# Optimization experiments

Measured on AMD Instinct MI355X. Metric: run time of the kernel, lower is better.

Reference implementation:

```python
import jax, jax.numpy as jnp
import numpy as np

EPS = 1e-5
N_HEADS = 8

def _layernorm(h, g, b):
    mu = jnp.mean(h, axis=-1, keepdims=True)
    var = jnp.mean((h - mu) ** 2, axis=-1, keepdims=True)
    return g * (h - mu) * jax.lax.rsqrt(var + EPS) + b

def _mlp_ln(x, W1, b1, W2, b2, g, beta):
    # Linear -> SiLU -> Linear -> LayerNorm (torch nn.Sequential processor)
    h = jax.nn.silu(x @ W1.T + b1)
    h = h @ W2.T + b2
    return _layernorm(h, g, beta)

def setup_inputs() -> dict:
    key = jax.random.key(0)
    ks = jax.random.split(key, 16)
    B, S, D = 4, 2048, 1024
    M, P, C = 128, 256, 512
    def lin(k, o, i):
        return (jax.random.normal(k, (o, i), jnp.float32) / np.sqrt(i)).astype(jnp.float32)
    inp = {}
    inp['x'] = jax.random.normal(ks[0], (B, S, D), jnp.float32)
    inp['scale_types'] = jax.random.randint(ks[1], (B, S), 0, 3)
    for name, dim, k1, k2 in [('mol', M, 2, 3), ('path', P, 4, 5), ('cell', C, 6, 7)]:
        inp[name + '_W1'] = lin(ks[k1], dim, D)
        inp[name + '_b1'] = jnp.zeros((dim,), jnp.float32)
        inp[name + '_W2'] = lin(ks[k2], dim, dim)
        inp[name + '_b2'] = jnp.zeros((dim,), jnp.float32)
        inp[name + '_g'] = jnp.ones((dim,), jnp.float32)
        inp[name + '_beta'] = jnp.zeros((dim,), jnp.float32)
    inp['int_W1'] = lin(ks[8], D, M + P + C)
    inp['int_b1'] = jnp.zeros((D,), jnp.float32)
    inp['int_W2'] = lin(ks[9], D, D)
    inp['int_b2'] = jnp.zeros((D,), jnp.float32)
    inp['int_g'] = jnp.ones((D,), jnp.float32)
    inp['int_beta'] = jnp.zeros((D,), jnp.float32)
    inp['attn_Wqkv'] = lin(ks[10], 3 * D, D)
    inp['attn_bqkv'] = jnp.zeros((3 * D,), jnp.float32)
    inp['attn_Wo'] = lin(ks[11], D, D)
    inp['attn_bo'] = jnp.zeros((D,), jnp.float32)
    inp['scale_w'] = jnp.ones((3,), jnp.float32) / 3.0
    return inp

def reference(x, scale_types,
              mol_W1, mol_b1, mol_W2, mol_b2, mol_g, mol_beta,
              path_W1, path_b1, path_W2, path_b2, path_g, path_beta,
              cell_W1, cell_b1, cell_W2, cell_b2, cell_g, cell_beta,
              int_W1, int_b1, int_W2, int_b2, int_g, int_beta,
              attn_Wqkv, attn_bqkv, attn_Wo, attn_bo, scale_w):
    B, S, D = x.shape
    # per-token routing: each token goes through exactly one expert; the
    # other two scale outputs are zeros (mask instead of Python loop).
    mol = _mlp_ln(x, mol_W1, mol_b1, mol_W2, mol_b2, mol_g, mol_beta) * (scale_types == 0)[..., None]
    path = _mlp_ln(x, path_W1, path_b1, path_W2, path_b2, path_g, path_beta) * (scale_types == 1)[..., None]
    cell = _mlp_ln(x, cell_W1, cell_b1, cell_W2, cell_b2, cell_g, cell_beta) * (scale_types == 2)[..., None]
    cat = jnp.concatenate([mol, path, cell], axis=-1)  # [B,S,M+P+C]
    integrated = _layernorm(jax.nn.silu(cat @ int_W1.T + int_b1) @ int_W2.T + int_b2, int_g, int_beta)
    # torch nn.MultiheadAttention (batch_first, self-attention)
    Dh = D // N_HEADS
    qkv = integrated @ attn_Wqkv.T + attn_bqkv  # [B,S,3D]
    q, k, v = jnp.split(qkv, 3, axis=-1)
    q = q.reshape(B, S, N_HEADS, Dh)
    k = k.reshape(B, S, N_HEADS, Dh)
    v = v.reshape(B, S, N_HEADS, Dh)
    scores = jnp.einsum('bqhd,bkhd->bhqk', q, k) / np.sqrt(Dh).astype(np.float32)
    attn = jax.nn.softmax(scores, axis=-1)
    o = jnp.einsum('bhqk,bkhd->bqhd', attn, v).reshape(B, S, D)
    attended = o @ attn_Wo.T + attn_bo
    w = jax.nn.softmax(scale_w, axis=0)
    final = integrated + w[0] * attended
    return (final, mol, path, cell)
```

## Files before the change

### kernel.cpp

```cpp
#include <hip/hip_runtime.h>
#include <cstdint>
#include <cstddef>

typedef unsigned short u16;
typedef unsigned int u32;
typedef short bf16x8 __attribute__((ext_vector_type(8)));
typedef float f32x4 __attribute__((ext_vector_type(4)));

__device__ __forceinline__ float bf2f(u16 u){
  union { u32 i; float f; } c; c.i = ((u32)u) << 16; return c.f;
}
__device__ __forceinline__ u16 f2bf(float f){
  union { float f; u32 i; } c; c.f = f;
  u32 r = c.i + 0x7FFFu + ((c.i >> 16) & 1u);
  return (u16)(r >> 16);
}
__device__ __forceinline__ void gload_lds16(const void* g, void* l){
  __builtin_amdgcn_global_load_lds(
      (const __attribute__((address_space(1))) u32*)g,
      (__attribute__((address_space(3))) u32*)l, 16, 0, 0);
}

struct ConvArgs {
  const float* src[11];
  u16* dst[11];
  u32 base[12];
};
__global__ __launch_bounds__(256)
void f32_to_bf16_multi(ConvArgs a){
  u32 i = blockIdx.x * 256 + threadIdx.x;
  if (i >= a.base[11]) return;
  int j = 0;
  #pragma unroll
  for (int k = 1; k < 11; ++k) j += (i >= a.base[k]);
  u32 li = i - a.base[j];
  const float4* s = (const float4*)a.src[j] + (size_t)li * 2;
  float4 va = s[0], vb = s[1];
  u16 o[8] = {f2bf(va.x),f2bf(va.y),f2bf(va.z),f2bf(va.w),
              f2bf(vb.x),f2bf(vb.y),f2bf(vb.z),f2bf(vb.w)};
  *(uint4*)(a.dst[j] + (size_t)li * 8) = *(const uint4*)o;
}

__global__ __launch_bounds__(256)
void concat3_f32(const float* __restrict__ a, const float* __restrict__ b,
                 const float* __restrict__ c, float* __restrict__ d){
  int i = blockIdx.x * 256 + threadIdx.x;
  if (i < 128) d[i] = a[i];
  else if (i < 384) d[i] = b[i - 128];
  else if (i < 896) d[i] = c[i - 384];
}

template<int EPI>
__device__ __forceinline__ void gemm_body(
    const u16* __restrict__ A, const u16* __restrict__ W,
    const float* __restrict__ bias, void* __restrict__ Cv,
    int N, int K, int lda, int ldc,
    const u16* __restrict__ I, const float* __restrict__ sw,
    int bx, int by)
{
  __shared__ __align__(16) u16 As[128*64];
  __shared__ __align__(16) u16 Bs[128*64];
  const int tid  = threadIdx.x;
  const int lane = tid & 63;
  const int wave = tid >> 6;
  const int wr = wave >> 1, wc = wave & 1;
  const int m0 = by * 128, n0 = bx * 128;

  f32x4 acc[4][4];
  #pragma unroll
  for (int r=0;r<4;++r)
    #pragma unroll
    for (int c=0;c<4;++c)
      #pragma unroll
      for (int e=0;e<4;++e) acc[r][c][e] = 0.f;

  int srow[4], soff[4];
  #pragma unroll
  for (int j=0;j<4;++j){
    int rr = (wave*4 + j)*8 + (lane>>3);
    srow[j] = rr;
    soff[j] = ((lane & 7) ^ (rr & 7)) * 8;
  }

  for (int k0 = 0; k0 < K; k0 += 64){
    #pragma unroll
    for (int j=0;j<4;++j){
      gload_lds16(A + (size_t)(m0 + srow[j])*lda + k0 + soff[j], As + (wave*4+j)*512);
      gload_lds16(W + (size_t)(n0 + srow[j])*K   + k0 + soff[j], Bs + (wave*4+j)*512);
    }
    __syncthreads();
    #pragma unroll
    for (int ks=0; ks<2; ++ks){
      bf16x8 af[4], bfr[4];
      #pragma unroll
      for (int r=0;r<4;++r){
        int row = wr*64 + r*16 + (lane&15);
        int cs  = (ks*4 + (lane>>4)) ^ (row & 7);
        af[r] = *(const bf16x8*)(As + row*64 + cs*8);
      }
      #pragma unroll
      for (int c=0;c<4;++c){
        int row = wc*64 + c*16 + (lane&15);
        int cs  = (ks*4 + (lane>>4)) ^ (row & 7);
        bfr[c] = *(const bf16x8*)(Bs + row*64 + cs*8);
      }
      #pragma unroll
      for (int r=0;r<4;++r)
        #pragma unroll
        for (int c=0;c<4;++c)
          acc[r][c] = __builtin_amdgcn_mfma_f32_16x16x32_bf16(af[r], bfr[c], acc[r][c], 0,0,0);
    }
    __syncthreads();
  }

  float w0 = 0.f;
  if (EPI == 2){
    float s0 = sw[0], s1 = sw[1], s2 = sw[2];
    float mx = fmaxf(s0, fmaxf(s1, s2));
    float e0 = __expf(s0-mx), e1 = __expf(s1-mx), e2 = __expf(s2-mx);
    w0 = e0 / (e0 + e1 + e2);
  }
  u16*   C16 = (u16*)Cv;
  float* C32 = (float*)Cv;
  #pragma unroll
  for (int c=0;c<4;++c){
    int col = n0 + wc*64 + c*16 + (lane&15);
    float bv = bias[col];
    #pragma unroll
    for (int r=0;r<4;++r){
      int rbase = m0 + wr*64 + r*16 + (lane>>4)*4;
      #pragma unroll
      for (int e=0;e<4;++e){
        int row = rbase + e;
        float v = acc[r][c][e] + bv;
        if (EPI == 1) v = v / (1.f + __expf(-v));
        if (EPI == 2){
          v = bf2f(I[(size_t)row*ldc + col]) + w0 * v;
          C32[(size_t)row*ldc + col] = v;
        } else {
          C16[(size_t)row*ldc + col] = f2bf(v);
        }
      }
    }
  }
}

template<int EPI>
__global__ __launch_bounds__(256, 2)
void gemm_bt(const u16* __restrict__ A, const u16* __restrict__ W,
             const float* __restrict__ bias, void* __restrict__ Cv,
             int N, int K, int lda, int ldc,
             const u16* __restrict__ I, const float* __restrict__ sw)
{
  gemm_body<EPI>(A, W, bias, Cv, N, K, lda, ldc, I, sw, blockIdx.x, blockIdx.y);
}

__global__ __launch_bounds__(256, 2)
void gemm_w2group(const u16* __restrict__ S1, u16* __restrict__ S2,
                  const u16* __restrict__ w0, const u16* __restrict__ w1,
                  const u16* __restrict__ w2, const float* __restrict__ b0,
                  const float* __restrict__ b1, const float* __restrict__ b2)
{
  int bx = blockIdx.x;
  if (bx < 64){
    gemm_body<0>(S1, w0, b0, S2, 128, 128, 896, 896, nullptr, nullptr, 0, bx);
  } else if (bx < 192){
    int l = bx - 64;
    gemm_body<0>(S1+128, w1, b1, S2+128, 256, 256, 896, 896, nullptr, nullptr, l>>6, l&63);
  } else {
    int l = bx - 192;
    gemm_body<0>(S1+384, w2, b2, S2+384, 512, 512, 896, 896, nullptr, nullptr, l>>6, l&63);
  }
}

template<int D>
__device__ __forceinline__ void ln_body_masked(
    u16* __restrict__ H, int ldh, const float* __restrict__ g,
    const float* __restrict__ beta, const int* __restrict__ st,
    int eid, float* __restrict__ outp)
{
  const int tid = threadIdx.x, lane = tid & 63, wave = tid >> 6;
  const int token = blockIdx.x * 4 + wave;
  constexpr int VPT = D / 64;
  float v[VPT];
  u16* row = H + (size_t)token * ldh + lane * VPT;
  #pragma unroll
  for (int i=0;i<VPT/2;++i){
    u32 u = ((const u32*)row)[i];
    v[2*i]   = bf2f((u16)(u & 0xFFFFu));
    v[2*i+1] = bf2f((u16)(u >> 16));
  }
  float s = 0.f;
  #pragma unroll
  for (int i=0;i<VPT;++i) s += v[i];
  #pragma unroll
  for (int off=1; off<64; off<<=1) s += __shfl_xor(s, off);
  float mu = s * (1.f / D);
  float q = 0.f;
  #pragma unroll
  for (int i=0;i<VPT;++i){ float d = v[i] - mu; q += d * d; }
  #pragma unroll
  for (int off=1; off<64; off<<=1) q += __shfl_xor(q, off);
  float rs = rsqrtf(q * (1.f / D) + 1e-5f);
  float msk = (st[token] == eid) ? 1.f : 0.f;
  #pragma unroll
  for (int i=0;i<VPT;++i){
    float gg = g[lane*VPT + i];
    float bb = beta[lane*VPT + i];
    float val = (gg * (v[i] - mu) * rs + bb) * msk;
    outp[(size_t)token * D + lane * VPT + i] = val;
    row[i] = f2bf(val);
  }
}

__global__ __launch_bounds__(256, 4)
void ln_expert(u16* __restrict__ S2,
               const float* __restrict__ g0, const float* __restrict__ be0,
               const float* __restrict__ g1, const float* __restrict__ be1,
               const float* __restrict__ g2, const float* __restrict__ be2,
               const int* __restrict__ st,
               float* __restrict__ o0, float* __restrict__ o1,
               float* __restrict__ o2)
{
  if (blockIdx.y == 0)      ln_body_masked<128>(S2,     896, g0, be0, st, 0, o0);
  else if (blockIdx.y == 1) ln_body_masked<256>(S2+128, 896, g1, be1, st, 1, o1);
  else                      ln_body_masked<512>(S2+384, 896, g2, be2, st, 2, o2);
}

__global__ __launch_bounds__(256, 4)
void ln_int(const u16* __restrict__ H, const float* __restrict__ g,
            const float* __restrict__ beta, u16* __restrict__ outp)
{
  const int tid = threadIdx.x, lane = tid & 63, wave = tid >> 6;
  const int token = blockIdx.x * 4 + wave;
  constexpr int D = 1024, VPT = 16;
  float v[VPT];
  const u16* row = H + (size_t)token * D + lane * VPT;
  #pragma unroll
  for (int i=0;i<VPT/2;++i){
    u32 u = ((const u32*)row)[i];
    v[2*i]   = bf2f((u16)(u & 0xFFFFu));
    v[2*i+1] = bf2f((u16)(u >> 16));
  }
  float s = 0.f;
  #pragma unroll
  for (int i=0;i<VPT;++i) s += v[i];
  #pragma unroll
  for (int off=1; off<64; off<<=1) s += __shfl_xor(s, off);
  float mu = s * (1.f / D);
  float q = 0.f;
  #pragma unroll
  for (int i=0;i<VPT;++i){ float d = v[i] - mu; q += d * d; }
  #pragma unroll
  for (int off=1; off<64; off<<=1) q += __shfl_xor(q, off);
  float rs = rsqrtf(q * (1.f / D) + 1e-5f);
  #pragma unroll
  for (int i=0;i<VPT;++i){
    float val = g[lane*VPT + i] * (v[i] - mu) * rs + beta[lane*VPT + i];
    outp[(size_t)token * D + lane * VPT + i] = f2bf(val);
  }
}

__global__ __launch_bounds__(256)
void transpose_v(const u16* __restrict__ qkv, u16* __restrict__ vt)
{
  __shared__ __align__(16) u16 T[64*72];
  const int tid = threadIdx.x;
  const int tt = blockIdx.x;
  const int dt = blockIdx.y;
  const int bh = blockIdx.z;
  const int b = bh >> 3, h = bh & 7;
  #pragma unroll
  for (int i=0;i<2;++i){
    int idx = tid + 256*i;
    int r = idx >> 3, c8 = idx & 7;
    const uint4* src = (const uint4*)(qkv + (size_t)(b*2048 + tt*64 + r)*3072
                                      + 2048 + h*128 + dt*64 + c8*8);
    *(uint4*)(T + r*72 + ((c8 ^ (r>>3)) & 7)*8) = *src;
  }
  __syncthreads();
  #pragma unroll
  for (int i=0;i<2;++i){
    int idx = tid + 256*i;
    int dr = idx >> 3, tc = idx & 7;
    u16 tmp[8];
    #pragma unroll
    for (int j=0;j<8;++j){
      int kap = tc*8 + j;
      int hp = kap >> 5, r2 = kap & 31;
      int srow = hp*32 + ((r2 & 1) ? 16 + (r2 >> 1) : (r2 >> 1));
      tmp[j] = T[srow*72 + (((dr>>3) ^ (srow>>3)) & 7)*8 + (dr & 7)];
    }
    *(uint4*)(vt + ((size_t)bh*128 + dt*64 + dr)*2048 + tt*64 + tc*8) = *(const uint4*)tmp;
  }
}

__global__ __launch_bounds__(256, 4)
void flash_attn(const u16* __restrict__ qkv, const u16* __restrict__ vt,
                u16* __restrict__ o)
{
  __shared__ __align__(16) u16 Ks[8192];
  __shared__ __align__(16) u16 Vs[8192];
  __shared__ __align__(16) u16 Ps[4*1024];
  const int tid = threadIdx.x, lane = tid & 63, wave = tid >> 6;
  const int b = blockIdx.z, h = blockIdx.y, q0 = blockIdx.x * 64;
  const float cl2   = 0.12751791892f;
  const float DEFER = 90.50966799187809f;

  bf16x8 qreg[4];
  {
    const u16* qrow = qkv + (size_t)(b*2048 + q0 + wave*16 + (lane&15))*3072
                      + h*128 + (lane>>4)*8;
    #pragma unroll
    for (int kk=0;kk<4;++kk) qreg[kk] = *(const bf16x8*)(qrow + kk*32);
  }
  asm volatile("s_waitcnt vmcnt(0)" ::: "memory");

  const u16* ksrc[4]; const u16* vsrc[4]; int cdst[4];
  #pragma unroll
  for (int i=0;i<4;++i){
    int cidx = (wave*4 + i)*64 + lane;
    int krow = cidx >> 4, kcs = cidx & 15;
    int kcsrc = (kcs & 8) | ((kcs & 7) ^ (krow & 7));
    ksrc[i] = qkv + (size_t)(b*2048 + krow)*3072 + h*128 + 1024 + kcsrc*8;
    int vd = cidx >> 3, vcs = cidx & 7;
    vsrc[i] = vt + ((size_t)(b*8 + h)*128 + vd)*2048 + (vcs ^ (vd & 7))*8;
    cdst[i] = cidx * 8;
  }

  auto stageK = [&](int kt){
    #pragma unroll
    for (int i=0;i<4;++i) gload_lds16(ksrc[i] + (size_t)kt*196608, Ks + cdst[i]);
  };
  auto stageV = [&](int kt){
    #pragma unroll
    for (int i=0;i<4;++i) gload_lds16(vsrc[i] + kt*64, Vs + cdst[i]);
  };

  f32x4 oacc[8];
  #pragma unroll
  for (int f=0;f<8;++f)
    #pragma unroll
    for (int e=0;e<4;++e) oacc[f][e] = 0.f;
  float m_run[4] = {-3e38f,-3e38f,-3e38f,-3e38f};
  float l_run[4] = {0.f,0.f,0.f,0.f};
  u16* PsW  = Ps + wave*1024;
  u32* PsW32 = (u32*)PsW;

  stageK(0);
  stageV(0);
  asm volatile("s_waitcnt vmcnt(4)" ::: "memory");
  __builtin_amdgcn_s_barrier();
  __builtin_amdgcn_sched_barrier(0);

  for (int kt=0; kt<32; ++kt){
    f32x4 s[4];
    #pragma unroll
    for (int cb=0;cb<4;++cb)
      #pragma unroll
      for (int e=0;e<4;++e) s[cb][e] = 0.f;
    __builtin_amdgcn_s_setprio(1);
    #pragma unroll
    for (int kk=0;kk<4;++kk){
      #pragma unroll
      for (int cb=0;cb<4;++cb){
        int row  = (lane&15) + 16*cb;
        int c    = kk*4 + (lane>>4);
        int slot = (c & 8) | ((c & 7) ^ (row & 7));
        bf16x8 bk = *(const bf16x8*)(Ks + row*128 + slot*8);
        s[cb] = __builtin_amdgcn_mfma_f32_16x16x32_bf16(qreg[kk], bk, s[cb], 0,0,0);
      }
    }
    __builtin_amdgcn_s_setprio(0);
    asm volatile("s_waitcnt lgkmcnt(0)" ::: "memory");
    __builtin_amdgcn_sched_barrier(0);
    __builtin_amdgcn_s_barrier();
    __builtin_amdgcn_sched_barrier(0);
    stageK((kt+1)&31);

    #pragma unroll
    for (int e=0;e<4;++e){
      float t0 = s[0][e], t1 = s[1][e], t2 = s[2][e], t3 = s[3][e];
      float lmx = fmaxf(fmaxf(t0,t1), fmaxf(t2,t3));
      if (__any(lmx > m_run[e] + DEFER)){
        float mx = lmx;
        #pragma unroll
        for (int off=1; off<16; off<<=1) mx = fmaxf(mx, __shfl_xor(mx, off));
        float mnew = fmaxf(m_run[e], mx);
        float a = exp2f((m_run[e] - mnew) * cl2);
        m_run[e] = mnew;
        l_run[e] *= a;
        #pragma unroll
        for (int f=0;f<8;++f) oacc[f][e] *= a;
      }
      float ms = m_run[e];
      float p0 = exp2f((t0 - ms)*cl2), p1 = exp2f((t1 - ms)*cl2);
      float p2 = exp2f((t2 - ms)*cl2), p3 = exp2f((t3 - ms)*cl2);
      l_run[e] += (p0 + p1) + (p2 + p3);
      u32 c01, c23;
      asm("v_cvt_pk_bf16_f32 %0, %1, %2" : "=v"(c01) : "v"(p0), "v"(p1));
      asm("v_cvt_pk_bf16_f32 %0, %1, %2" : "=v"(c23) : "v"(p2), "v"(p3));
      int prow = (lane>>4)*4 + e;
      u32* base = PsW32 + prow*32;
      int j01 = lane & 15;
      int j23 = 16 + (lane & 15);
      base[((((j01>>2) ^ (prow&7)) & 7)<<2) | (j01&3)] = c01;
      base[((((j23>>2) ^ (prow&7)) & 7)<<2) | (j23&3)] = c23;
    }

    asm volatile("s_waitcnt vmcnt(4)" ::: "memory");
    __builtin_amdgcn_sched_barrier(0);
    __builtin_amdgcn_s_barrier();
    __builtin_amdgcn_sched_barrier(0);

    __builtin_amdgcn_s_setprio(1);
    #pragma unroll
    for (int kk=0;kk<2;++kk){
      int prow = lane & 15;
      int pc   = kk*4 + (lane>>4);
      bf16x8 pa = *(const bf16x8*)(PsW + prow*64 + ((pc ^ (prow & 7)) & 7)*8);
      #pragma unroll
      for (int f=0;f<8;++f){
        int d = f*16 + (lane&15);
        int c = kk*4 + (lane>>4);
        bf16x8 vb = *(const bf16x8*)(Vs + d*64 + (c ^ (d & 7))*8);
        oacc[f] = __builtin_amdgcn_mfma_f32_16x16x32_bf16(pa, vb, oacc[f], 0,0,0);
      }
    }
    __builtin_amdgcn_s_setprio(0);
    asm volatile("s_waitcnt lgkmcnt(0) vmcnt(0)" ::: "memory");
    __builtin_amdgcn_sched_barrier(0);
    __builtin_amdgcn_s_barrier();
    __builtin_amdgcn_sched_barrier(0);
    if (kt + 1 < 32) stageV(kt+1);
  }

  #pragma unroll
  for (int e=0;e<4;++e){
    float l = l_run[e];
    #pragma unroll
    for (int off=1; off<16; off<<=1) l += __shfl_xor(l, off);
    l_run[e] = 1.f / l;
  }
  #pragma unroll
  for (int f=0;f<8;++f)
    #pragma unroll
    for (int e=0;e<4;++e){
      int row = q0 + wave*16 + (lane>>4)*4 + e;
      int col = h*128 + f*16 + (lane&15);
      o[(size_t)(b*2048 + row)*1024 + col] = f2bf(oacc[f][e] * l_run[e]);
    }
}

extern "C" void kernel_launch(void* const* d_in, const int* in_sizes, int n_in,
                              void* d_out, int out_size, void* d_ws, size_t ws_size,
                              hipStream_t stream)
{
  const float* x         = (const float*)d_in[0];
  const int*   stypes    = (const int*)d_in[1];
  const float* mol_W1    = (const float*)d_in[2];
  const float* mol_b1    = (const float*)d_in[3];
  const float* mol_W2    = (const float*)d_in[4];
  const float* mol_b2    = (const float*)d_in[5];
  const float* mol_g     = (const float*)d_in[6];
  const float* mol_beta  = (const float*)d_in[7];
  const float* path_W1   = (const float*)d_in[8];
  const float* path_b1   = (const float*)d_in[9];
  const float* path_W2   = (const float*)d_in[10];
  const float* path_b2   = (const float*)d_in[11];
  const float* path_g    = (const float*)d_in[12];
  const float* path_beta = (const float*)d_in[13];
  const float* cell_W1   = (const float*)d_in[14];
  const float* cell_b1   = (const float*)d_in[15];
  const float* cell_W2   = (const float*)d_in[16];
  const float* cell_b2   = (const float*)d_in[17];
  const float* cell_g    = (const float*)d_in[18];
  const float* cell_beta = (const float*)d_in[19];
  const float* int_W1    = (const float*)d_in[20];
  const float* int_b1    = (const float*)d_in[21];
  const float* int_W2    = (const float*)d_in[22];
  const float* int_b2    = (const float*)d_in[23];
  const float* int_g     = (const float*)d_in[24];
  const float* int_beta  = (const float*)d_in[25];
  const float* attn_Wqkv = (const float*)d_in[26];
  const float* attn_bqkv = (const float*)d_in[27];
  const float* attn_Wo   = (const float*)d_in[28];
  const float* attn_bo   = (const float*)d_in[29];
  const float* scale_w   = (const float*)d_in[30];

  float* out_final = (float*)d_out;
  float* out_mol   = out_final + 8388608;
  float* out_path  = out_mol   + 1048576;
  float* out_cell  = out_path  + 2097152;

  u16* ws    = (u16*)d_ws;
  u16* qkv   = ws;
  u16* integ = qkv   + 25165824;
  u16* S1    = integ + 8388608;
  u16* S2    = S1    + 8388608;
  u16* wb    = S2    + 8388608;
  u16* xb    = qkv;

  u16* w1f    = wb;
  u16* molW2b = w1f    + 917504;
  u16* pathW2b= molW2b + 16384;
  u16* cellW2b= pathW2b+ 65536;
  u16* intW1b = cellW2b+ 262144;
  u16* intW2b = intW1b + 917504;
  u16* qkvWb  = intW2b + 1048576;
  u16* woWb   = qkvWb  + 3145728;
  float* fbias= (float*)(woWb + 1048576);

  dim3 blk(256);

  ConvArgs ca;
  const float* srcs[11] = {x, mol_W1, path_W1, cell_W1, mol_W2, path_W2,
                           cell_W2, int_W1, int_W2, attn_Wqkv, attn_Wo};
  u16* dsts[11] = {xb, w1f, w1f + 131072, w1f + 393216, molW2b, pathW2b,
                   cellW2b, intW1b, intW2b, qkvWb, woWb};
  u32 n8s[11] = {1048576, 16384, 32768, 65536, 2048, 8192,
                 32768, 114688, 131072, 393216, 131072};
  u32 acc8 = 0;
  for (int i=0;i<11;++i){ ca.src[i]=srcs[i]; ca.dst[i]=dsts[i]; ca.base[i]=acc8; acc8+=n8s[i]; }
  ca.base[11] = acc8;
  f32_to_bf16_multi<<<(acc8 + 255)/256, blk, 0, stream>>>(ca);
  concat3_f32<<<4, blk, 0, stream>>>(mol_b1, path_b1, cell_b1, fbias);

  gemm_bt<1><<<dim3(7,64), blk, 0, stream>>>(xb, w1f, fbias, S1, 896, 1024, 1024, 896, nullptr, nullptr);
  gemm_w2group<<<448, blk, 0, stream>>>(S1, S2, molW2b, pathW2b, cellW2b,
                                        mol_b2, path_b2, cell_b2);
  ln_expert<<<dim3(2048,3), blk, 0, stream>>>(S2, mol_g, mol_beta, path_g,
                                              path_beta, cell_g, cell_beta,
                                              stypes, out_mol, out_path, out_cell);

  gemm_bt<1><<<dim3(8,64), blk, 0, stream>>>(S2, intW1b, int_b1, S1, 1024, 896,  896,  1024, nullptr, nullptr);
  gemm_bt<0><<<dim3(8,64), blk, 0, stream>>>(S1, intW2b, int_b2, S2, 1024, 1024, 1024, 1024, nullptr, nullptr);
  ln_int<<<2048, blk, 0, stream>>>(S2, int_g, int_beta, integ);

  gemm_bt<0><<<dim3(24,64), blk, 0, stream>>>(integ, qkvWb, attn_bqkv, qkv, 3072, 1024, 1024, 3072, nullptr, nullptr);
  transpose_v<<<dim3(32,2,32), blk, 0, stream>>>(qkv, S2);
  flash_attn<<<dim3(32,8,4), blk, 0, stream>>>(qkv, S2, S1);

  gemm_bt<2><<<dim3(8,64), blk, 0, stream>>>(S1, woWb, attn_bo, out_final, 1024, 1024, 1024, 1024, integ, scale_w);
}
```

Before: 329.0 us.

## Compact tokens per expert and run expert MLP GEMMs on routed rows only

A new single-block kernel builds per-expert token index lists and counts from scale_types. The expert W1 and W2 GEMMs then gather only routed rows and scatter results back, skipping tiles past each expert's count. Before, all three experts ran over every token and the results were masked afterwards. Rows for unrouted tokens in S2 are no longer written, so the masked layernorm now clamps inputs to keep stale values from producing NaN. Separately, gemm_bt remaps its block index so consecutive tiles land on the same XCD, which should improve cache locality.

```diff
diff --git a/kernel.cpp b/kernel.cpp
--- a/kernel.cpp
+++ b/kernel.cpp
@@ -42,29 +42,52 @@
 }
 
 __global__ __launch_bounds__(256)
-void concat3_f32(const float* __restrict__ a, const float* __restrict__ b,
-                 const float* __restrict__ c, float* __restrict__ d){
-  int i = blockIdx.x * 256 + threadIdx.x;
-  if (i < 128) d[i] = a[i];
-  else if (i < 384) d[i] = b[i - 128];
-  else if (i < 896) d[i] = c[i - 384];
-}
-
-template<int EPI>
+void route_compact(const int* __restrict__ st, int* __restrict__ idx,
+                   int* __restrict__ counts){
+  __shared__ int cnt[3][257];
+  const int tid = threadIdx.x;
+  int t[32];
+  #pragma unroll
+  for (int i=0;i<32;++i) t[i] = st[tid*32 + i];
+  int c0=0,c1=0,c2=0;
+  #pragma unroll
+  for (int i=0;i<32;++i){ c0 += (t[i]==0); c1 += (t[i]==1); c2 += (t[i]==2); }
+  cnt[0][tid+1]=c0; cnt[1][tid+1]=c1; cnt[2][tid+1]=c2;
+  if (tid < 3) cnt[tid][0] = 0;
+  __syncthreads();
+  if (tid < 3){
+    int acc = 0;
+    for (int i=1;i<=256;++i){ acc += cnt[tid][i]; cnt[tid][i] = acc; }
+    counts[tid] = acc;
+  }
+  __syncthreads();
+  int b0 = cnt[0][tid], b1 = cnt[1][tid], b2 = cnt[2][tid];
+  #pragma unroll
+  for (int i=0;i<32;++i){
+    int tok = tid*32 + i;
+    if (t[i]==0)      idx[b0++] = tok;
+    else if (t[i]==1) idx[8192  + b1++] = tok;
+    else              idx[16384 + b2++] = tok;
+  }
+}
+
+template<int EPI, int MODE>
 __device__ __forceinline__ void gemm_body(
     const u16* __restrict__ A, const u16* __restrict__ W,
     const float* __restrict__ bias, void* __restrict__ Cv,
     int N, int K, int lda, int ldc,
     const u16* __restrict__ I, const float* __restrict__ sw,
-    int bx, int by)
-{
+    int bx, int by, const int* __restrict__ ridx, int count)
+{
+  const int m0 = by * 128, n0 = bx * 128;
+  if (MODE && m0 >= count) return;
+
   __shared__ __align__(16) u16 As[128*64];
   __shared__ __align__(16) u16 Bs[128*64];
   const int tid  = threadIdx.x;
   const int lane = tid & 63;
   const int wave = tid >> 6;
   const int wr = wave >> 1, wc = wave & 1;
-  const int m0 = by * 128, n0 = bx * 128;
 
   f32x4 acc[4][4];
   #pragma unroll
@@ -74,19 +97,23 @@
       #pragma unroll
       for (int e=0;e<4;++e) acc[r][c][e] = 0.f;
 
-  int srow[4], soff[4];
+  int srow[4], soff[4], arow[4];
   #pragma unroll
   for (int j=0;j<4;++j){
     int rr = (wave*4 + j)*8 + (lane>>3);
     srow[j] = rr;
     soff[j] = ((lane & 7) ^ (rr & 7)) * 8;
+    int gr = m0 + rr;
+    if (MODE == 1)      arow[j] = ridx[gr < count ? gr : count-1];
+    else if (MODE == 2) arow[j] = gr < count ? gr : count-1;
+    else                arow[j] = gr;
   }
 
   for (int k0 = 0; k0 < K; k0 += 64){
     #pragma unroll
     for (int j=0;j<4;++j){
-      gload_lds16(A + (size_t)(m0 + srow[j])*lda + k0 + soff[j], As + (wave*4+j)*512);
-      gload_lds16(W + (size_t)(n0 + srow[j])*K   + k0 + soff[j], Bs + (wave*4+j)*512);
+      gload_lds16(A + (size_t)arow[j]*lda + k0 + soff[j], As + (wave*4+j)*512);
+      gload_lds16(W + (size_t)(n0 + srow[j])*K + k0 + soff[j], Bs + (wave*4+j)*512);
     }
     __syncthreads();
     #pragma unroll
@@ -134,11 +161,13 @@
         int row = rbase + e;
         float v = acc[r][c][e] + bv;
         if (EPI == 1) v = v / (1.f + __expf(-v));
+        if (MODE && row >= count) continue;
+        int crow = (MODE == 2) ? ridx[row] : row;
         if (EPI == 2){
-          v = bf2f(I[(size_t)row*ldc + col]) + w0 * v;
-          C32[(size_t)row*ldc + col] = v;
+          v = bf2f(I[(size_t)crow*ldc + col]) + w0 * v;
+          C32[(size_t)crow*ldc + col] = v;
         } else {
-          C16[(size_t)row*ldc + col] = f2bf(v);
+          C16[(size_t)crow*ldc + col] = f2bf(v);
         }
       }
     }
@@ -152,24 +181,60 @@
              int N, int K, int lda, int ldc,
              const u16* __restrict__ I, const float* __restrict__ sw)
 {
-  gemm_body<EPI>(A, W, bias, Cv, N, K, lda, ldc, I, sw, blockIdx.x, blockIdx.y);
+  int gx = gridDim.x;
+  int nwg = gx * gridDim.y;
+  int flat = blockIdx.y * gx + blockIdx.x;
+  int q = nwg >> 3;
+  int swz = (flat & 7) * q + (flat >> 3);
+  gemm_body<EPI,0>(A, W, bias, Cv, N, K, lda, ldc, I, sw,
+                   swz % gx, swz / gx, nullptr, 0);
 }
 
 __global__ __launch_bounds__(256, 2)
-void gemm_w2group(const u16* __restrict__ S1, u16* __restrict__ S2,
+void gemm_w1group(const u16* __restrict__ xb,
+                  u16* __restrict__ s1_0, u16* __restrict__ s1_1, u16* __restrict__ s1_2,
                   const u16* __restrict__ w0, const u16* __restrict__ w1,
-                  const u16* __restrict__ w2, const float* __restrict__ b0,
-                  const float* __restrict__ b1, const float* __restrict__ b2)
+                  const u16* __restrict__ w2,
+                  const float* __restrict__ b0, const float* __restrict__ b1,
+                  const float* __restrict__ b2,
+                  const int* __restrict__ idx, const int* __restrict__ counts)
 {
   int bx = blockIdx.x;
   if (bx < 64){
-    gemm_body<0>(S1, w0, b0, S2, 128, 128, 896, 896, nullptr, nullptr, 0, bx);
+    gemm_body<1,1>(xb, w0, b0, s1_0, 128, 1024, 1024, 128, nullptr, nullptr,
+                   0, bx, idx, counts[0]);
   } else if (bx < 192){
     int l = bx - 64;
-    gemm_body<0>(S1+128, w1, b1, S2+128, 256, 256, 896, 896, nullptr, nullptr, l>>6, l&63);
+    gemm_body<1,1>(xb, w1, b1, s1_1, 256, 1024, 1024, 256, nullptr, nullptr,
+                   l>>6, l&63, idx + 8192, counts[1]);
   } else {
     int l = bx - 192;
-    gemm_body<0>(S1+384, w2, b2, S2+384, 512, 512, 896, 896, nullptr, nullptr, l>>6, l&63);
+    gemm_body<1,1>(xb, w2, b2, s1_2, 512, 1024, 1024, 512, nullptr, nullptr,
+                   l>>6, l&63, idx + 16384, counts[2]);
+  }
+}
+
+__global__ __launch_bounds__(256, 2)
+void gemm_w2group(const u16* __restrict__ s1_0, const u16* __restrict__ s1_1,
+                  const u16* __restrict__ s1_2, u16* __restrict__ S2,
+                  const u16* __restrict__ w0, const u16* __restrict__ w1,
+                  const u16* __restrict__ w2,
+                  const float* __restrict__ b0, const float* __restrict__ b1,
+                  const float* __restrict__ b2,
+                  const int* __restrict__ idx, const int* __restrict__ counts)
+{
+  int bx = blockIdx.x;
+  if (bx < 64){
+    gemm_body<0,2>(s1_0, w0, b0, S2, 128, 128, 128, 896, nullptr, nullptr,
+                   0, bx, idx, counts[0]);
+  } else if (bx < 192){
+    int l = bx - 64;
+    gemm_body<0,2>(s1_1, w1, b1, S2 + 128, 256, 256, 256, 896, nullptr, nullptr,
+                   l>>6, l&63, idx + 8192, counts[1]);
+  } else {
+    int l = bx - 192;
+    gemm_body<0,2>(s1_2, w2, b2, S2 + 384, 512, 512, 512, 896, nullptr, nullptr,
+                   l>>6, l&63, idx + 16384, counts[2]);
   }
 }
 
@@ -190,6 +255,8 @@
     v[2*i]   = bf2f((u16)(u & 0xFFFFu));
     v[2*i+1] = bf2f((u16)(u >> 16));
   }
+  #pragma unroll
+  for (int i=0;i<VPT;++i) v[i] = fminf(fmaxf(v[i], -1e15f), 1e15f);
   float s = 0.f;
   #pragma unroll
   for (int i=0;i<VPT;++i) s += v[i];
@@ -501,22 +568,29 @@
   u16* wb    = S2    + 8388608;
   u16* xb    = qkv;
 
-  u16* w1f    = wb;
-  u16* molW2b = w1f    + 917504;
-  u16* pathW2b= molW2b + 16384;
-  u16* cellW2b= pathW2b+ 65536;
-  u16* intW1b = cellW2b+ 262144;
-  u16* intW2b = intW1b + 917504;
-  u16* qkvWb  = intW2b + 1048576;
-  u16* woWb   = qkvWb  + 3145728;
-  float* fbias= (float*)(woWb + 1048576);
+  u16* molW1b  = wb;
+  u16* pathW1b = molW1b + 131072;
+  u16* cellW1b = pathW1b + 262144;
+  u16* molW2b  = cellW1b + 524288;
+  u16* pathW2b = molW2b + 16384;
+  u16* cellW2b = pathW2b + 65536;
+  u16* intW1b  = cellW2b + 262144;
+  u16* intW2b  = intW1b + 917504;
+  u16* qkvWb   = intW2b + 1048576;
+  u16* woWb    = qkvWb  + 3145728;
+  int* ridx    = (int*)(woWb + 1048576);
+  int* rcounts = ridx + 24576;
+
+  u16* s1_0 = S1;
+  u16* s1_1 = S1 + 8192*128;
+  u16* s1_2 = s1_1 + (size_t)8192*256;
 
   dim3 blk(256);
 
   ConvArgs ca;
   const float* srcs[11] = {x, mol_W1, path_W1, cell_W1, mol_W2, path_W2,
                            cell_W2, int_W1, int_W2, attn_Wqkv, attn_Wo};
-  u16* dsts[11] = {xb, w1f, w1f + 131072, w1f + 393216, molW2b, pathW2b,
+  u16* dsts[11] = {xb, molW1b, pathW1b, cellW1b, molW2b, pathW2b,
                    cellW2b, intW1b, intW2b, qkvWb, woWb};
   u32 n8s[11] = {1048576, 16384, 32768, 65536, 2048, 8192,
                  32768, 114688, 131072, 393216, 131072};
@@ -524,11 +598,14 @@
   for (int i=0;i<11;++i){ ca.src[i]=srcs[i]; ca.dst[i]=dsts[i]; ca.base[i]=acc8; acc8+=n8s[i]; }
   ca.base[11] = acc8;
   f32_to_bf16_multi<<<(acc8 + 255)/256, blk, 0, stream>>>(ca);
-  concat3_f32<<<4, blk, 0, stream>>>(mol_b1, path_b1, cell_b1, fbias);
-
-  gemm_bt<1><<<dim3(7,64), blk, 0, stream>>>(xb, w1f, fbias, S1, 896, 1024, 1024, 896, nullptr, nullptr);
-  gemm_w2group<<<448, blk, 0, stream>>>(S1, S2, molW2b, pathW2b, cellW2b,
-                                        mol_b2, path_b2, cell_b2);
+  route_compact<<<1, blk, 0, stream>>>(stypes, ridx, rcounts);
+
+  gemm_w1group<<<448, blk, 0, stream>>>(xb, s1_0, s1_1, s1_2,
+                                        molW1b, pathW1b, cellW1b,
+                                        mol_b1, path_b1, cell_b1, ridx, rcounts);
+  gemm_w2group<<<448, blk, 0, stream>>>(s1_0, s1_1, s1_2, S2,
+                                        molW2b, pathW2b, cellW2b,
+                                        mol_b2, path_b2, cell_b2, ridx, rcounts);
   ln_expert<<<dim3(2048,3), blk, 0, stream>>>(S2, mol_g, mol_beta, path_g,
                                               path_beta, cell_g, cell_beta,
                                               stypes, out_mol, out_path, out_cell);
```

Result: slower. 343.7 us (+4.5%).
